# Kernel optimization log

Measured on AMD Instinct MI355X. Metric: run time of the kernel, lower is better.

## Reference

```python
import jax, jax.numpy as jnp
import numpy as np

VOL = 64          # self.vol_size
SPACE = 0.2       # space_size (cubic), space_center = 0
IMG = 255.0       # normalization constant in the source (2*u/255 - 1)


def setup_inputs() -> dict:
    key = jax.random.key(0)
    ks = jax.random.split(key, 5)
    B, V, C, Hf, Wf = 2, 4, 32, 64, 64
    features = jax.random.normal(ks[0], (B, V, C, Hf, Wf), jnp.float32)
    # near-identity rotations, cameras ~0.5m away, focal ~200, principal point 128
    camera_R = jnp.eye(3, dtype=jnp.float32)[None, None] + 0.01 * jax.random.normal(ks[1], (B, V, 3, 3), jnp.float32)
    camera_T = jnp.array([0.0, 0.0, 0.5], jnp.float32) + 0.01 * jax.random.normal(ks[2], (B, V, 3), jnp.float32)
    K0 = jnp.array([[200.0, 0.0, 128.0], [0.0, 200.0, 128.0], [0.0, 0.0, 1.0]], jnp.float32)
    Kmask = jnp.array([[1.0, 0.0, 1.0], [0.0, 1.0, 1.0], [0.0, 0.0, 0.0]], jnp.float32)
    camera_K = K0[None, None] + 0.5 * jax.random.normal(ks[3], (B, V, 3, 3), jnp.float32) * Kmask
    root_world = 0.01 * jax.random.normal(ks[4], (B, 3), jnp.float32)
    return dict(features=features, camera_R=camera_R, camera_T=camera_T,
                camera_K=camera_K, root_world=root_world)


def _bilinear_sample(feat, x, y):
    """PyTorch F.grid_sample, mode=bilinear, padding=zeros, align_corners=False.
    feat: [N,C,H,W]; x,y: [N,P] pixel-space coords (already unnormalized).
    Returns [N,C,P]."""
    N, C, H, W = feat.shape
    x0 = jnp.floor(x); y0 = jnp.floor(y)
    x1 = x0 + 1.0;     y1 = y0 + 1.0
    wx1 = x - x0; wx0 = 1.0 - wx1
    wy1 = y - y0; wy0 = 1.0 - wy1
    feat_flat = feat.reshape(N, C, H * W)

    def gather(xi, yi, w):
        valid = (xi >= 0) & (xi <= W - 1) & (yi >= 0) & (yi <= H - 1)
        xi_c = jnp.clip(xi, 0, W - 1).astype(jnp.int32)
        yi_c = jnp.clip(yi, 0, H - 1).astype(jnp.int32)
        idx = yi_c * W + xi_c                                   # [N,P]
        vals = jnp.take_along_axis(feat_flat, idx[:, None, :], axis=2)  # [N,C,P]
        return vals * (w * valid.astype(feat.dtype))[:, None, :]

    return (gather(x0, y0, wx0 * wy0) + gather(x1, y0, wx1 * wy0)
            + gather(x0, y1, wx0 * wy1) + gather(x1, y1, wx1 * wy1))


def reference(features, camera_R, camera_T, camera_K, root_world):
    B, V, C, Hf, Wf = features.shape
    D = VOL
    # _build_grid: 64^3 points, xyz order, spanning SPACE around center 0
    r = jnp.arange(D, dtype=jnp.float32)
    z, y, x = jnp.meshgrid(r, r, r, indexing='ij')
    grid = jnp.stack([x, y, z], axis=0) / (D - 1)               # [3,D,D,D]
    pts = ((grid - 0.5) * SPACE).reshape(3, -1).T               # [P,3], P = D^3
    # relative camera translation: new_T = R @ root + T
    new_T = jnp.einsum('bvij,bj->bvi', camera_R, root_world) + camera_T
    # project: pts_cam = pts @ R^T + T  -> [B,V,P,3]
    pts_cam = jnp.einsum('pj,bvij->bvpi', pts, camera_R) + new_T[:, :, None, :]
    zc = jnp.maximum(pts_cam[..., 2], 1e-5)
    fx = camera_K[:, :, 0, 0][..., None]; fy = camera_K[:, :, 1, 1][..., None]
    cx = camera_K[:, :, 0, 2][..., None]; cy = camera_K[:, :, 1, 2][..., None]
    u = pts_cam[..., 0] * fx / zc + cx
    v = pts_cam[..., 1] * fy / zc + cy
    u_n = 2.0 * u / IMG - 1.0
    v_n = 2.0 * v / IMG - 1.0
    # unnormalize (align_corners=False): ix = ((g+1)*W - 1)/2
    px = ((u_n + 1.0) * Wf - 1.0) * 0.5
    py = ((v_n + 1.0) * Hf - 1.0) * 0.5
    feat_bv = features.reshape(B * V, C, Hf, Wf)
    vol = _bilinear_sample(feat_bv, px.reshape(B * V, -1), py.reshape(B * V, -1))  # [BV,C,P]
    vol = vol.reshape(B, V, C, D, D, D).mean(axis=1)            # average over views
    return vol
```

## Files before the change

### kernel.cpp

```cpp
#include <hip/hip_runtime.h>

#define B_   2
#define V_   4
#define C_   32
#define HW_  4096
#define D_   64
#define P_   (D_*D_*D_)
#define SCL_ (64.0f/255.0f)

#define TXv_ 16
#define TYv_ 4
#define TZv_ 2
#define WCAP_ 10
#define HCAP_ 6
#define SLOTS_   64
#define SSTRIDE_ 80

typedef _Float16 half2v __attribute__((ext_vector_type(2)));
typedef __fp16  fp16x2 __attribute__((ext_vector_type(2)));

union Corner32 { uint4 u[2]; half2v h[8]; };
union H2U { half2v h; fp16x2 f; unsigned int u; };

__global__ __launch_bounds__(256) void tx_kernel(const float* __restrict__ in,
                                                 unsigned int* __restrict__ out) {
    __shared__ float tile[32][65];
    const int bv  = blockIdx.x >> 6;
    const int hw0 = (blockIdx.x & 63) << 6;
    const int t   = threadIdx.x;
    const float* src = in + (size_t)bv * C_ * HW_ + hw0;
#pragma unroll
    for (int i = 0; i < 8; ++i) {
        int e = t + (i << 8);
        tile[e >> 6][e & 63] = src[(e >> 6) * HW_ + (e & 63)];
    }
    __syncthreads();
    unsigned int* dst = out + ((size_t)bv * HW_ + hw0) * (C_ / 2);
#pragma unroll
    for (int i = 0; i < 4; ++i) {
        int idx = t + (i << 8);
        int c  = (idx << 1) & 31;
        int hw = idx >> 4;
        half2v v = { (_Float16)tile[c][hw], (_Float16)tile[c + 1][hw] };
        dst[idx] = *(unsigned int*)&v;
    }
}

__global__ __launch_bounds__(256, 6) void vol_kernel(
    const unsigned char* __restrict__ feat,
    const float* __restrict__ Rm,
    const float* __restrict__ Tm,
    const float* __restrict__ Km,
    const float* __restrict__ root,
    float* __restrict__ out)
{
    __shared__ __align__(16) float cam[4][20];
    __shared__ __align__(16) int   srect[4][8];
    __shared__ __align__(16) unsigned char sfeat[4][SLOTS_ * SSTRIDE_];

    const int t = threadIdx.x;
    const int b = blockIdx.x >> 11;
    const int tile = blockIdx.x & 2047;
    const int gx0 = (tile & 3) << 4;
    const int gy0 = ((tile >> 2) & 15) << 2;
    const int gz0 = (tile >> 6) << 1;

    if (t < 32) {
        const int v = t & 3, c = t >> 2;
        const int bv = b * V_ + v;
        const float* Rb = Rm + bv * 9;
        const float* Tb = Tm + bv * 3;
        const float* Kb = Km + bv * 9;
        const float rx = root[b*3+0], ry = root[b*3+1], rz = root[b*3+2];
        const float r00=Rb[0], r01=Rb[1], r02=Rb[2];
        const float r10=Rb[3], r11=Rb[4], r12=Rb[5];
        const float r20=Rb[6], r21=Rb[7], r22=Rb[8];
        const float t0 = r00*rx + r01*ry + r02*rz + Tb[0];
        const float t1 = r10*rx + r11*ry + r12*rz + Tb[1];
        const float t2 = r20*rx + r21*ry + r22*rz + Tb[2];
        const float fx = Kb[0] * SCL_, fy = Kb[4] * SCL_;
        const float cx = Kb[2] * SCL_ - 0.5f, cy = Kb[5] * SCL_ - 0.5f;

        const float X = ((float)(gx0 + (c & 1) * (TXv_-1)) * (1.0f/63.0f) - 0.5f) * 0.2f;
        const float Y = ((float)(gy0 + ((c >> 1) & 1) * (TYv_-1)) * (1.0f/63.0f) - 0.5f) * 0.2f;
        const float Z = ((float)(gz0 + (c >> 2) * (TZv_-1)) * (1.0f/63.0f) - 0.5f) * 0.2f;
        const float xc = r00*X + r01*Y + r02*Z + t0;
        const float yc = r10*X + r11*Y + r12*Z + t1;
        float zc       = r20*X + r21*Y + r22*Z + t2;
        zc = fmaxf(zc, 1e-5f);
        const float inv = 1.0f / zc;
        float px = (xc * inv) * fx + cx;
        float py = (yc * inv) * fy + cy;

        float pxmn = px, pxmx = px, pymn = py, pymx = py;
#pragma unroll
        for (int m = 4; m <= 16; m <<= 1) {
            pxmn = fminf(pxmn, __shfl_xor(pxmn, m));
            pxmx = fmaxf(pxmx, __shfl_xor(pxmx, m));
            pymn = fminf(pymn, __shfl_xor(pymn, m));
            pymx = fmaxf(pymx, __shfl_xor(pymx, m));
        }
        if (c == 0) {
            cam[v][0] = r00; cam[v][1] = r01; cam[v][2] = r02; cam[v][3] = t0;
            cam[v][4] = r10; cam[v][5] = r11; cam[v][6] = r12; cam[v][7] = t1;
            cam[v][8] = r20; cam[v][9] = r21; cam[v][10] = r22; cam[v][11] = t2;
            cam[v][12] = fx; cam[v][13] = fy; cam[v][14] = cx; cam[v][15] = cy;
            int rx0 = (int)floorf(pxmn); rx0 = max(0, min(63, rx0));
            int rx1 = (int)floorf(pxmx) + 1; rx1 = max(rx0, min(63, rx1));
            const int W = min(rx1 - rx0 + 1, WCAP_);
            int ry0 = (int)floorf(pymn); ry0 = max(0, min(63, ry0));
            int ry1 = (int)floorf(pymx) + 1; ry1 = max(ry0, min(63, ry1));
            const int H = min(ry1 - ry0 + 1, HCAP_);
            srect[v][0] = rx0; srect[v][1] = ry0; srect[v][2] = W; srect[v][3] = H;
            srect[v][4] = 65536 / W + 1;
            srect[v][5] = W * H * 4;
        }
    }
    __syncthreads();

    const int bvb = b * V_;
#pragma unroll
    for (int v = 0; v < 4; ++v) {
        const int nch = srect[v][5];
        if (t < nch) {
            const int rx0 = srect[v][0], ry0 = srect[v][1];
            const int W = srect[v][2], M = srect[v][4];
            const int part = t & 3, pi = t >> 2;
            const int dy = (pi * M) >> 16;
            const int dx = pi - dy * W;
            const unsigned char* src = feat + (size_t)(bvb + v) * HW_ * 64;
            const uint4 val = *(const uint4*)(src
                + (size_t)(((ry0 + dy) << 6) + rx0 + dx) * 64 + part * 16);
            *(uint4*)&sfeat[v][pi * SSTRIDE_ + part * 16] = val;
        }
    }
    __syncthreads();

    const int h = t & 1;
    const int vx = t >> 1;
    const float X = ((float)(gx0 + (vx & 15)) * (1.0f/63.0f) - 0.5f) * 0.2f;
    const float Y = ((float)(gy0 + ((vx >> 4) & 3)) * (1.0f/63.0f) - 0.5f) * 0.2f;
    const float Z = ((float)(gz0 + (vx >> 6)) * (1.0f/63.0f) - 0.5f) * 0.2f;

    const half2v z2 = { (_Float16)0.0f, (_Float16)0.0f };
    half2v acc[8];
#pragma unroll
    for (int j = 0; j < 8; ++j) acc[j] = z2;

#pragma unroll
    for (int v = 0; v < 4; ++v) {
        const float4 cA = *(const float4*)&cam[v][0];
        const float4 cB = *(const float4*)&cam[v][4];
        const float4 cC = *(const float4*)&cam[v][8];
        const float4 cK = *(const float4*)&cam[v][12];
        const int rx0 = srect[v][0], ry0 = srect[v][1], W = srect[v][2];

        const float xc = cA.x*X + cA.y*Y + cA.z*Z + cA.w;
        const float yc = cB.x*X + cB.y*Y + cB.z*Z + cB.w;
        float zc       = cC.x*X + cC.y*Y + cC.z*Z + cC.w;
        zc = fmaxf(zc, 1e-5f);
        const float inv = 1.0f / zc;
        const float px = (xc * inv) * cK.x + cK.z;
        const float py = (yc * inv) * cK.y + cK.w;

        const float x0f = floorf(px), y0f = floorf(py);
        const float wx1 = px - x0f, wx0 = 1.0f - wx1;
        const float wy1 = py - y0f, wy0 = 1.0f - wy1;
        const float x1f = x0f + 1.0f, y1f = y0f + 1.0f;
        const float vx0 = (x0f >= 0.0f && x0f <= 63.0f) ? 0.25f : 0.0f;
        const float vx1 = (x1f >= 0.0f && x1f <= 63.0f) ? 0.25f : 0.0f;
        const float vy0 = (y0f >= 0.0f && y0f <= 63.0f) ? 1.0f : 0.0f;
        const float vy1 = (y1f >= 0.0f && y1f <= 63.0f) ? 1.0f : 0.0f;
        const float w00 = wx0*wy0*vx0*vy0, w01 = wx1*wy0*vx1*vy0;
        const float w10 = wx0*wy1*vx0*vy1, w11 = wx1*wy1*vx1*vy1;
        H2U u0, u1, u2, u3;
        u0.f = __builtin_amdgcn_cvt_pkrtz(w00, w00);
        u1.f = __builtin_amdgcn_cvt_pkrtz(w01, w01);
        u2.f = __builtin_amdgcn_cvt_pkrtz(w10, w10);
        u3.f = __builtin_amdgcn_cvt_pkrtz(w11, w11);

        const int x0c = (int)fminf(fmaxf(x0f, 0.0f), 63.0f);
        const int x1c = (int)fminf(fmaxf(x1f, 0.0f), 63.0f);
        const int y0c = (int)fminf(fmaxf(y0f, 0.0f), 63.0f);
        const int y1c = (int)fminf(fmaxf(y1f, 0.0f), 63.0f);
        const int dx0 = x0c - rx0, dx1 = x1c - rx0;
        const int r0 = (y0c - ry0) * W, r1 = (y1c - ry0) * W;
        const int o00 = (r0 + dx0) * SSTRIDE_, o01 = (r0 + dx1) * SSTRIDE_;
        const int o10 = (r1 + dx0) * SSTRIDE_, o11 = (r1 + dx1) * SSTRIDE_;

        const unsigned char* vb = &sfeat[v][0] + (h << 5);
        Corner32 c00, c01, c10, c11;
        c00.u[0] = *(const uint4*)(vb + o00); c00.u[1] = *(const uint4*)(vb + o00 + 16);
        c01.u[0] = *(const uint4*)(vb + o01); c01.u[1] = *(const uint4*)(vb + o01 + 16);
        c10.u[0] = *(const uint4*)(vb + o10); c10.u[1] = *(const uint4*)(vb + o10 + 16);
        c11.u[0] = *(const uint4*)(vb + o11); c11.u[1] = *(const uint4*)(vb + o11 + 16);
#pragma unroll
        for (int j = 0; j < 8; ++j) {
            acc[j] += c00.h[j] * u0.h;
            acc[j] += c01.h[j] * u1.h;
            acc[j] += c10.h[j] * u2.h;
            acc[j] += c11.h[j] * u3.h;
        }
    }

    const int gx = gx0 + (vx & 15);
    const int gy = gy0 + ((vx >> 4) & 3);
    const int gz = gz0 + (vx >> 6);
    const int p = (((gz << 6) + gy) << 6) + gx;
    float* ob = out + ((size_t)(b * C_) + (h << 4)) * P_ + p;
#pragma unroll
    for (int j = 0; j < 8; ++j) {
        __builtin_nontemporal_store((float)acc[j].x, ob + (size_t)(2*j  ) * P_);
        __builtin_nontemporal_store((float)acc[j].y, ob + (size_t)(2*j+1) * P_);
    }
}

__global__ __launch_bounds__(256) void vol_fallback(
    const float* __restrict__ feat,
    const float* __restrict__ Rm, const float* __restrict__ Tm,
    const float* __restrict__ Km, const float* __restrict__ root,
    float* __restrict__ out)
{
    const int b = blockIdx.x >> 10;
    const int p = ((blockIdx.x & 1023) << 8) | threadIdx.x;
    const int xi = p & 63, yi = (p >> 6) & 63, zi = p >> 12;
    const float X = ((float)xi * (1.0f/63.0f) - 0.5f) * 0.2f;
    const float Y = ((float)yi * (1.0f/63.0f) - 0.5f) * 0.2f;
    const float Z = ((float)zi * (1.0f/63.0f) - 0.5f) * 0.2f;
    float acc[C_];
#pragma unroll
    for (int c = 0; c < C_; ++c) acc[c] = 0.0f;
    const float rx = root[b*3+0], ry = root[b*3+1], rz = root[b*3+2];
#pragma unroll
    for (int v = 0; v < V_; ++v) {
        const int bv = b * V_ + v;
        const float* Rb = Rm + bv * 9; const float* Tb = Tm + bv * 3;
        const float* Kb = Km + bv * 9;
        const float r00=Rb[0], r01=Rb[1], r02=Rb[2];
        const float r10=Rb[3], r11=Rb[4], r12=Rb[5];
        const float r20=Rb[6], r21=Rb[7], r22=Rb[8];
        const float t0 = r00*rx + r01*ry + r02*rz + Tb[0];
        const float t1 = r10*rx + r11*ry + r12*rz + Tb[1];
        const float t2 = r20*rx + r21*ry + r22*rz + Tb[2];
        const float xc = r00*X + r01*Y + r02*Z + t0;
        const float yc = r10*X + r11*Y + r12*Z + t1;
        float zc       = r20*X + r21*Y + r22*Z + t2;
        zc = fmaxf(zc, 1e-5f);
        const float inv = 1.0f / zc;
        const float px = xc * (Kb[0]*SCL_) * inv + (Kb[2]*SCL_ - 0.5f);
        const float py = yc * (Kb[4]*SCL_) * inv + (Kb[5]*SCL_ - 0.5f);
        const float x0f = floorf(px), y0f = floorf(py);
        const float wx1 = px - x0f, wx0 = 1.0f - wx1;
        const float wy1 = py - y0f, wy0 = 1.0f - wy1;
        const float x1f = x0f + 1.0f, y1f = y0f + 1.0f;
        const float vx0 = (x0f >= 0.0f && x0f <= 63.0f) ? 1.0f : 0.0f;
        const float vx1 = (x1f >= 0.0f && x1f <= 63.0f) ? 1.0f : 0.0f;
        const float vy0 = (y0f >= 0.0f && y0f <= 63.0f) ? 1.0f : 0.0f;
        const float vy1 = (y1f >= 0.0f && y1f <= 63.0f) ? 1.0f : 0.0f;
        const float w00 = wx0*wy0*vx0*vy0, w01 = wx1*wy0*vx1*vy0;
        const float w10 = wx0*wy1*vx0*vy1, w11 = wx1*wy1*vx1*vy1;
        const int x0c = (int)fminf(fmaxf(x0f, 0.0f), 63.0f);
        const int x1c = (int)fminf(fmaxf(x1f, 0.0f), 63.0f);
        const int y0c = (int)fminf(fmaxf(y0f, 0.0f), 63.0f);
        const int y1c = (int)fminf(fmaxf(y1f, 0.0f), 63.0f);
        const float* fb = feat + (size_t)bv * C_ * HW_;
        const int i00 = y0c*64 + x0c, i01 = y0c*64 + x1c;
        const int i10 = y1c*64 + x0c, i11 = y1c*64 + x1c;
#pragma unroll
        for (int c = 0; c < C_; ++c) {
            const float* f = fb + c * HW_;
            acc[c] += w00*f[i00] + w01*f[i01] + w10*f[i10] + w11*f[i11];
        }
    }
    float* ob = out + (size_t)b * C_ * P_ + p;
#pragma unroll
    for (int c = 0; c < C_; ++c) ob[(size_t)c * P_] = acc[c] * 0.25f;
}

extern "C" void kernel_launch(void* const* d_in, const int* in_sizes, int n_in,
                              void* d_out, int out_size, void* d_ws, size_t ws_size,
                              hipStream_t stream) {
    const float* feat = (const float*)d_in[0];
    const float* Rm   = (const float*)d_in[1];
    const float* Tm   = (const float*)d_in[2];
    const float* Km   = (const float*)d_in[3];
    const float* root = (const float*)d_in[4];
    float* out = (float*)d_out;

    const size_t need = (size_t)B_ * V_ * HW_ * C_ * sizeof(_Float16);
    if (ws_size >= need) {
        unsigned int* ftx = (unsigned int*)d_ws;
        tx_kernel<<<B_ * V_ * 64, 256, 0, stream>>>(feat, ftx);
        vol_kernel<<<B_ * 2048, 256, 0, stream>>>(
            (const unsigned char*)ftx, Rm, Tm, Km, root, out);
    } else {
        vol_fallback<<<B_ * P_ / 256, 256, 0, stream>>>(feat, Rm, Tm, Km, root, out);
    }
}
```

Before: 97.58 us.

## Gather bilinear corners directly from global memory instead of LDS staging

New measurement: 100.9 us. 1.03x slower.

```diff
diff --git a/kernel.cpp b/kernel.cpp
--- a/kernel.cpp
+++ b/kernel.cpp
@@ -11,10 +11,6 @@
 #define TXv_ 16
 #define TYv_ 4
 #define TZv_ 2
-#define WCAP_ 10
-#define HCAP_ 6
-#define SLOTS_   64
-#define SSTRIDE_ 80
 
 typedef _Float16 half2v __attribute__((ext_vector_type(2)));
 typedef __fp16  fp16x2 __attribute__((ext_vector_type(2)));
@@ -46,7 +42,7 @@
     }
 }
 
-__global__ __launch_bounds__(256, 6) void vol_kernel(
+__global__ __launch_bounds__(256, 4) void vol_kernel(
     const unsigned char* __restrict__ feat,
     const float* __restrict__ Rm,
     const float* __restrict__ Tm,
@@ -54,10 +50,6 @@
     const float* __restrict__ root,
     float* __restrict__ out)
 {
-    __shared__ __align__(16) float cam[4][20];
-    __shared__ __align__(16) int   srect[4][8];
-    __shared__ __align__(16) unsigned char sfeat[4][SLOTS_ * SSTRIDE_];
-
     const int t = threadIdx.x;
     const int b = blockIdx.x >> 11;
     const int tile = blockIdx.x & 2047;
@@ -65,13 +57,25 @@
     const int gy0 = ((tile >> 2) & 15) << 2;
     const int gz0 = (tile >> 6) << 1;
 
-    if (t < 32) {
-        const int v = t & 3, c = t >> 2;
+    const int h = t & 1;
+    const int vx = t >> 1;
+    const float X = ((float)(gx0 + (vx & 15)) * (1.0f/63.0f) - 0.5f) * 0.2f;
+    const float Y = ((float)(gy0 + ((vx >> 4) & 3)) * (1.0f/63.0f) - 0.5f) * 0.2f;
+    const float Z = ((float)(gz0 + (vx >> 6)) * (1.0f/63.0f) - 0.5f) * 0.2f;
+
+    const float rx = root[b*3+0], ry = root[b*3+1], rz = root[b*3+2];
+
+    const half2v z2 = { (_Float16)0.0f, (_Float16)0.0f };
+    half2v acc[8];
+#pragma unroll
+    for (int j = 0; j < 8; ++j) acc[j] = z2;
+
+#pragma unroll
+    for (int v = 0; v < 4; ++v) {
         const int bv = b * V_ + v;
         const float* Rb = Rm + bv * 9;
         const float* Tb = Tm + bv * 3;
         const float* Kb = Km + bv * 9;
-        const float rx = root[b*3+0], ry = root[b*3+1], rz = root[b*3+2];
         const float r00=Rb[0], r01=Rb[1], r02=Rb[2];
         const float r10=Rb[3], r11=Rb[4], r12=Rb[5];
         const float r20=Rb[6], r21=Rb[7], r22=Rb[8];
@@ -81,87 +85,13 @@
         const float fx = Kb[0] * SCL_, fy = Kb[4] * SCL_;
         const float cx = Kb[2] * SCL_ - 0.5f, cy = Kb[5] * SCL_ - 0.5f;
 
-        const float X = ((float)(gx0 + (c & 1) * (TXv_-1)) * (1.0f/63.0f) - 0.5f) * 0.2f;
-        const float Y = ((float)(gy0 + ((c >> 1) & 1) * (TYv_-1)) * (1.0f/63.0f) - 0.5f) * 0.2f;
-        const float Z = ((float)(gz0 + (c >> 2) * (TZv_-1)) * (1.0f/63.0f) - 0.5f) * 0.2f;
         const float xc = r00*X + r01*Y + r02*Z + t0;
         const float yc = r10*X + r11*Y + r12*Z + t1;
         float zc       = r20*X + r21*Y + r22*Z + t2;
         zc = fmaxf(zc, 1e-5f);
         const float inv = 1.0f / zc;
-        float px = (xc * inv) * fx + cx;
-        float py = (yc * inv) * fy + cy;
-
-        float pxmn = px, pxmx = px, pymn = py, pymx = py;
-#pragma unroll
-        for (int m = 4; m <= 16; m <<= 1) {
-            pxmn = fminf(pxmn, __shfl_xor(pxmn, m));
-            pxmx = fmaxf(pxmx, __shfl_xor(pxmx, m));
-            pymn = fminf(pymn, __shfl_xor(pymn, m));
-            pymx = fmaxf(pymx, __shfl_xor(pymx, m));
-        }
-        if (c == 0) {
-            cam[v][0] = r00; cam[v][1] = r01; cam[v][2] = r02; cam[v][3] = t0;
-            cam[v][4] = r10; cam[v][5] = r11; cam[v][6] = r12; cam[v][7] = t1;
-            cam[v][8] = r20; cam[v][9] = r21; cam[v][10] = r22; cam[v][11] = t2;
-            cam[v][12] = fx; cam[v][13] = fy; cam[v][14] = cx; cam[v][15] = cy;
-            int rx0 = (int)floorf(pxmn); rx0 = max(0, min(63, rx0));
-            int rx1 = (int)floorf(pxmx) + 1; rx1 = max(rx0, min(63, rx1));
-            const int W = min(rx1 - rx0 + 1, WCAP_);
-            int ry0 = (int)floorf(pymn); ry0 = max(0, min(63, ry0));
-            int ry1 = (int)floorf(pymx) + 1; ry1 = max(ry0, min(63, ry1));
-            const int H = min(ry1 - ry0 + 1, HCAP_);
-            srect[v][0] = rx0; srect[v][1] = ry0; srect[v][2] = W; srect[v][3] = H;
-            srect[v][4] = 65536 / W + 1;
-            srect[v][5] = W * H * 4;
-        }
-    }
-    __syncthreads();
-
-    const int bvb = b * V_;
-#pragma unroll
-    for (int v = 0; v < 4; ++v) {
-        const int nch = srect[v][5];
-        if (t < nch) {
-            const int rx0 = srect[v][0], ry0 = srect[v][1];
-            const int W = srect[v][2], M = srect[v][4];
-            const int part = t & 3, pi = t >> 2;
-            const int dy = (pi * M) >> 16;
-            const int dx = pi - dy * W;
-            const unsigned char* src = feat + (size_t)(bvb + v) * HW_ * 64;
-            const uint4 val = *(const uint4*)(src
-                + (size_t)(((ry0 + dy) << 6) + rx0 + dx) * 64 + part * 16);
-            *(uint4*)&sfeat[v][pi * SSTRIDE_ + part * 16] = val;
-        }
-    }
-    __syncthreads();
-
-    const int h = t & 1;
-    const int vx = t >> 1;
-    const float X = ((float)(gx0 + (vx & 15)) * (1.0f/63.0f) - 0.5f) * 0.2f;
-    const float Y = ((float)(gy0 + ((vx >> 4) & 3)) * (1.0f/63.0f) - 0.5f) * 0.2f;
-    const float Z = ((float)(gz0 + (vx >> 6)) * (1.0f/63.0f) - 0.5f) * 0.2f;
-
-    const half2v z2 = { (_Float16)0.0f, (_Float16)0.0f };
-    half2v acc[8];
-#pragma unroll
-    for (int j = 0; j < 8; ++j) acc[j] = z2;
-
-#pragma unroll
-    for (int v = 0; v < 4; ++v) {
-        const float4 cA = *(const float4*)&cam[v][0];
-        const float4 cB = *(const float4*)&cam[v][4];
-        const float4 cC = *(const float4*)&cam[v][8];
-        const float4 cK = *(const float4*)&cam[v][12];
-        const int rx0 = srect[v][0], ry0 = srect[v][1], W = srect[v][2];
-
-        const float xc = cA.x*X + cA.y*Y + cA.z*Z + cA.w;
-        const float yc = cB.x*X + cB.y*Y + cB.z*Z + cB.w;
-        float zc       = cC.x*X + cC.y*Y + cC.z*Z + cC.w;
-        zc = fmaxf(zc, 1e-5f);
-        const float inv = 1.0f / zc;
-        const float px = (xc * inv) * cK.x + cK.z;
-        const float py = (yc * inv) * cK.y + cK.w;
+        const float px = (xc * inv) * fx + cx;
+        const float py = (yc * inv) * fy + cy;
 
         const float x0f = floorf(px), y0f = floorf(py);
         const float wx1 = px - x0f, wx0 = 1.0f - wx1;
@@ -183,17 +113,15 @@
         const int x1c = (int)fminf(fmaxf(x1f, 0.0f), 63.0f);
         const int y0c = (int)fminf(fmaxf(y0f, 0.0f), 63.0f);
         const int y1c = (int)fminf(fmaxf(y1f, 0.0f), 63.0f);
-        const int dx0 = x0c - rx0, dx1 = x1c - rx0;
-        const int r0 = (y0c - ry0) * W, r1 = (y1c - ry0) * W;
-        const int o00 = (r0 + dx0) * SSTRIDE_, o01 = (r0 + dx1) * SSTRIDE_;
-        const int o10 = (r1 + dx0) * SSTRIDE_, o11 = (r1 + dx1) * SSTRIDE_;
-
-        const unsigned char* vb = &sfeat[v][0] + (h << 5);
+
+        const unsigned char* vb = feat + (size_t)bv * HW_ * 64 + (h << 5);
+        const int i00 = ((y0c << 6) + x0c) << 6, i01 = ((y0c << 6) + x1c) << 6;
+        const int i10 = ((y1c << 6) + x0c) << 6, i11 = ((y1c << 6) + x1c) << 6;
         Corner32 c00, c01, c10, c11;
-        c00.u[0] = *(const uint4*)(vb + o00); c00.u[1] = *(const uint4*)(vb + o00 + 16);
-        c01.u[0] = *(const uint4*)(vb + o01); c01.u[1] = *(const uint4*)(vb + o01 + 16);
-        c10.u[0] = *(const uint4*)(vb + o10); c10.u[1] = *(const uint4*)(vb + o10 + 16);
-        c11.u[0] = *(const uint4*)(vb + o11); c11.u[1] = *(const uint4*)(vb + o11 + 16);
+        c00.u[0] = *(const uint4*)(vb + i00); c00.u[1] = *(const uint4*)(vb + i00 + 16);
+        c01.u[0] = *(const uint4*)(vb + i01); c01.u[1] = *(const uint4*)(vb + i01 + 16);
+        c10.u[0] = *(const uint4*)(vb + i10); c10.u[1] = *(const uint4*)(vb + i10 + 16);
+        c11.u[0] = *(const uint4*)(vb + i11); c11.u[1] = *(const uint4*)(vb + i11 + 16);
 #pragma unroll
         for (int j = 0; j < 8; ++j) {
             acc[j] += c00.h[j] * u0.h;
```

## Process two z-slices per thread to amortize per-block camera and feature staging

Applied to the files above, without the earlier changes.

New measurement: 95.64 us. -2.0%, faster.

```diff
diff --git a/kernel.cpp b/kernel.cpp
--- a/kernel.cpp
+++ b/kernel.cpp
@@ -10,11 +10,12 @@
 
 #define TXv_ 16
 #define TYv_ 4
-#define TZv_ 2
+#define TZv_ 4
 #define WCAP_ 10
 #define HCAP_ 6
 #define SLOTS_   64
 #define SSTRIDE_ 80
+#define STEP_ (0.2f/63.0f)
 
 typedef _Float16 half2v __attribute__((ext_vector_type(2)));
 typedef __fp16  fp16x2 __attribute__((ext_vector_type(2)));
@@ -46,7 +47,51 @@
     }
 }
 
-__global__ __launch_bounds__(256, 6) void vol_kernel(
+__device__ __forceinline__ void gather_blend(
+    const unsigned char* __restrict__ vb,
+    float px, float py, int rx0, int ry0, int W,
+    half2v* __restrict__ acc)
+{
+    const float x0f = floorf(px), y0f = floorf(py);
+    const float wx1 = px - x0f, wx0 = 1.0f - wx1;
+    const float wy1 = py - y0f, wy0 = 1.0f - wy1;
+    const float x1f = x0f + 1.0f, y1f = y0f + 1.0f;
+    const float vx0 = (x0f >= 0.0f && x0f <= 63.0f) ? 0.25f : 0.0f;
+    const float vx1 = (x1f >= 0.0f && x1f <= 63.0f) ? 0.25f : 0.0f;
+    const float vy0 = (y0f >= 0.0f && y0f <= 63.0f) ? 1.0f : 0.0f;
+    const float vy1 = (y1f >= 0.0f && y1f <= 63.0f) ? 1.0f : 0.0f;
+    const float w00 = wx0*wy0*vx0*vy0, w01 = wx1*wy0*vx1*vy0;
+    const float w10 = wx0*wy1*vx0*vy1, w11 = wx1*wy1*vx1*vy1;
+    H2U u0, u1, u2, u3;
+    u0.f = __builtin_amdgcn_cvt_pkrtz(w00, w00);
+    u1.f = __builtin_amdgcn_cvt_pkrtz(w01, w01);
+    u2.f = __builtin_amdgcn_cvt_pkrtz(w10, w10);
+    u3.f = __builtin_amdgcn_cvt_pkrtz(w11, w11);
+
+    const int x0c = (int)fminf(fmaxf(x0f, 0.0f), 63.0f);
+    const int x1c = (int)fminf(fmaxf(x1f, 0.0f), 63.0f);
+    const int y0c = (int)fminf(fmaxf(y0f, 0.0f), 63.0f);
+    const int y1c = (int)fminf(fmaxf(y1f, 0.0f), 63.0f);
+    const int dx0 = x0c - rx0, dx1 = x1c - rx0;
+    const int r0 = (y0c - ry0) * W, r1 = (y1c - ry0) * W;
+    const int o00 = (r0 + dx0) * SSTRIDE_, o01 = (r0 + dx1) * SSTRIDE_;
+    const int o10 = (r1 + dx0) * SSTRIDE_, o11 = (r1 + dx1) * SSTRIDE_;
+
+    Corner32 c00, c01, c10, c11;
+    c00.u[0] = *(const uint4*)(vb + o00); c00.u[1] = *(const uint4*)(vb + o00 + 16);
+    c01.u[0] = *(const uint4*)(vb + o01); c01.u[1] = *(const uint4*)(vb + o01 + 16);
+    c10.u[0] = *(const uint4*)(vb + o10); c10.u[1] = *(const uint4*)(vb + o10 + 16);
+    c11.u[0] = *(const uint4*)(vb + o11); c11.u[1] = *(const uint4*)(vb + o11 + 16);
+#pragma unroll
+    for (int j = 0; j < 8; ++j) {
+        acc[j] += c00.h[j] * u0.h;
+        acc[j] += c01.h[j] * u1.h;
+        acc[j] += c10.h[j] * u2.h;
+        acc[j] += c11.h[j] * u3.h;
+    }
+}
+
+__global__ __launch_bounds__(256, 4) void vol_kernel(
     const unsigned char* __restrict__ feat,
     const float* __restrict__ Rm,
     const float* __restrict__ Tm,
@@ -59,11 +104,11 @@
     __shared__ __align__(16) unsigned char sfeat[4][SLOTS_ * SSTRIDE_];
 
     const int t = threadIdx.x;
-    const int b = blockIdx.x >> 11;
-    const int tile = blockIdx.x & 2047;
+    const int b = blockIdx.x >> 10;
+    const int tile = blockIdx.x & 1023;
     const int gx0 = (tile & 3) << 4;
     const int gy0 = ((tile >> 2) & 15) << 2;
-    const int gz0 = (tile >> 6) << 1;
+    const int gz0 = (tile >> 6) << 2;
 
     if (t < 32) {
         const int v = t & 3, c = t >> 2;
@@ -81,14 +126,14 @@
         const float fx = Kb[0] * SCL_, fy = Kb[4] * SCL_;
         const float cx = Kb[2] * SCL_ - 0.5f, cy = Kb[5] * SCL_ - 0.5f;
 
-        const float X = ((float)(gx0 + (c & 1) * (TXv_-1)) * (1.0f/63.0f) - 0.5f) * 0.2f;
-        const float Y = ((float)(gy0 + ((c >> 1) & 1) * (TYv_-1)) * (1.0f/63.0f) - 0.5f) * 0.2f;
-        const float Z = ((float)(gz0 + (c >> 2) * (TZv_-1)) * (1.0f/63.0f) - 0.5f) * 0.2f;
+        const float X = (float)(gx0 + (c & 1) * (TXv_-1)) * STEP_ - 0.1f;
+        const float Y = (float)(gy0 + ((c >> 1) & 1) * (TYv_-1)) * STEP_ - 0.1f;
+        const float Z = (float)(gz0 + (c >> 2) * (TZv_-1)) * STEP_ - 0.1f;
         const float xc = r00*X + r01*Y + r02*Z + t0;
         const float yc = r10*X + r11*Y + r12*Z + t1;
         float zc       = r20*X + r21*Y + r22*Z + t2;
         zc = fmaxf(zc, 1e-5f);
-        const float inv = 1.0f / zc;
+        const float inv = __builtin_amdgcn_rcpf(zc);
         float px = (xc * inv) * fx + cx;
         float py = (yc * inv) * fy + cy;
 
@@ -105,6 +150,8 @@
             cam[v][4] = r10; cam[v][5] = r11; cam[v][6] = r12; cam[v][7] = t1;
             cam[v][8] = r20; cam[v][9] = r21; cam[v][10] = r22; cam[v][11] = t2;
             cam[v][12] = fx; cam[v][13] = fy; cam[v][14] = cx; cam[v][15] = cy;
+            const float dZ = 2.0f * STEP_;
+            cam[v][16] = r02 * dZ; cam[v][17] = r12 * dZ; cam[v][18] = r22 * dZ;
             int rx0 = (int)floorf(pxmn); rx0 = max(0, min(63, rx0));
             int rx1 = (int)floorf(pxmx) + 1; rx1 = max(rx0, min(63, rx1));
             const int W = min(rx1 - rx0 + 1, WCAP_);
@@ -138,14 +185,14 @@
 
     const int h = t & 1;
     const int vx = t >> 1;
-    const float X = ((float)(gx0 + (vx & 15)) * (1.0f/63.0f) - 0.5f) * 0.2f;
-    const float Y = ((float)(gy0 + ((vx >> 4) & 3)) * (1.0f/63.0f) - 0.5f) * 0.2f;
-    const float Z = ((float)(gz0 + (vx >> 6)) * (1.0f/63.0f) - 0.5f) * 0.2f;
-
-    const half2v z2 = { (_Float16)0.0f, (_Float16)0.0f };
-    half2v acc[8];
-#pragma unroll
-    for (int j = 0; j < 8; ++j) acc[j] = z2;
+    const float X = (float)(gx0 + (vx & 15)) * STEP_ - 0.1f;
+    const float Y = (float)(gy0 + ((vx >> 4) & 3)) * STEP_ - 0.1f;
+    const float Z = (float)(gz0 + (vx >> 6)) * STEP_ - 0.1f;
+
+    const half2v z2h = { (_Float16)0.0f, (_Float16)0.0f };
+    half2v accA[8], accB[8];
+#pragma unroll
+    for (int j = 0; j < 8; ++j) { accA[j] = z2h; accB[j] = z2h; }
 
 #pragma unroll
     for (int v = 0; v < 4; ++v) {
@@ -153,54 +200,24 @@
         const float4 cB = *(const float4*)&cam[v][4];
         const float4 cC = *(const float4*)&cam[v][8];
         const float4 cK = *(const float4*)&cam[v][12];
+        const float dxz = cam[v][16], dyz = cam[v][17], dzz = cam[v][18];
         const int rx0 = srect[v][0], ry0 = srect[v][1], W = srect[v][2];
-
-        const float xc = cA.x*X + cA.y*Y + cA.z*Z + cA.w;
-        const float yc = cB.x*X + cB.y*Y + cB.z*Z + cB.w;
-        float zc       = cC.x*X + cC.y*Y + cC.z*Z + cC.w;
-        zc = fmaxf(zc, 1e-5f);
-        const float inv = 1.0f / zc;
-        const float px = (xc * inv) * cK.x + cK.z;
-        const float py = (yc * inv) * cK.y + cK.w;
-
-        const float x0f = floorf(px), y0f = floorf(py);
-        const float wx1 = px - x0f, wx0 = 1.0f - wx1;
-        const float wy1 = py - y0f, wy0 = 1.0f - wy1;
-        const float x1f = x0f + 1.0f, y1f = y0f + 1.0f;
-        const float vx0 = (x0f >= 0.0f && x0f <= 63.0f) ? 0.25f : 0.0f;
-        const float vx1 = (x1f >= 0.0f && x1f <= 63.0f) ? 0.25f : 0.0f;
-        const float vy0 = (y0f >= 0.0f && y0f <= 63.0f) ? 1.0f : 0.0f;
-        const float vy1 = (y1f >= 0.0f && y1f <= 63.0f) ? 1.0f : 0.0f;
-        const float w00 = wx0*wy0*vx0*vy0, w01 = wx1*wy0*vx1*vy0;
-        const float w10 = wx0*wy1*vx0*vy1, w11 = wx1*wy1*vx1*vy1;
-        H2U u0, u1, u2, u3;
-        u0.f = __builtin_amdgcn_cvt_pkrtz(w00, w00);
-        u1.f = __builtin_amdgcn_cvt_pkrtz(w01, w01);
-        u2.f = __builtin_amdgcn_cvt_pkrtz(w10, w10);
-        u3.f = __builtin_amdgcn_cvt_pkrtz(w11, w11);
-
-        const int x0c = (int)fminf(fmaxf(x0f, 0.0f), 63.0f);
-        const int x1c = (int)fminf(fmaxf(x1f, 0.0f), 63.0f);
-        const int y0c = (int)fminf(fmaxf(y0f, 0.0f), 63.0f);
-        const int y1c = (int)fminf(fmaxf(y1f, 0.0f), 63.0f);
-        const int dx0 = x0c - rx0, dx1 = x1c - rx0;
-        const int r0 = (y0c - ry0) * W, r1 = (y1c - ry0) * W;
-        const int o00 = (r0 + dx0) * SSTRIDE_, o01 = (r0 + dx1) * SSTRIDE_;
-        const int o10 = (r1 + dx0) * SSTRIDE_, o11 = (r1 + dx1) * SSTRIDE_;
-
         const unsigned char* vb = &sfeat[v][0] + (h << 5);
-        Corner32 c00, c01, c10, c11;
-        c00.u[0] = *(const uint4*)(vb + o00); c00.u[1] = *(const uint4*)(vb + o00 + 16);
-        c01.u[0] = *(const uint4*)(vb + o01); c01.u[1] = *(const uint4*)(vb + o01 + 16);
-        c10.u[0] = *(const uint4*)(vb + o10); c10.u[1] = *(const uint4*)(vb + o10 + 16);
-        c11.u[0] = *(const uint4*)(vb + o11); c11.u[1] = *(const uint4*)(vb + o11 + 16);
-#pragma unroll
-        for (int j = 0; j < 8; ++j) {
-            acc[j] += c00.h[j] * u0.h;
-            acc[j] += c01.h[j] * u1.h;
-            acc[j] += c10.h[j] * u2.h;
-            acc[j] += c11.h[j] * u3.h;
-        }
+
+        const float xcA = cA.x*X + cA.y*Y + cA.z*Z + cA.w;
+        const float ycA = cB.x*X + cB.y*Y + cB.z*Z + cB.w;
+        const float zcA = cC.x*X + cC.y*Y + cC.z*Z + cC.w;
+        const float xcB = xcA + dxz, ycB = ycA + dyz, zcB = zcA + dzz;
+
+        const float invA = __builtin_amdgcn_rcpf(fmaxf(zcA, 1e-5f));
+        const float invB = __builtin_amdgcn_rcpf(fmaxf(zcB, 1e-5f));
+        const float pxA = (xcA * invA) * cK.x + cK.z;
+        const float pyA = (ycA * invA) * cK.y + cK.w;
+        const float pxB = (xcB * invB) * cK.x + cK.z;
+        const float pyB = (ycB * invB) * cK.y + cK.w;
+
+        gather_blend(vb, pxA, pyA, rx0, ry0, W, accA);
+        gather_blend(vb, pxB, pyB, rx0, ry0, W, accB);
     }
 
     const int gx = gx0 + (vx & 15);
@@ -210,8 +227,10 @@
     float* ob = out + ((size_t)(b * C_) + (h << 4)) * P_ + p;
 #pragma unroll
     for (int j = 0; j < 8; ++j) {
-        __builtin_nontemporal_store((float)acc[j].x, ob + (size_t)(2*j  ) * P_);
-        __builtin_nontemporal_store((float)acc[j].y, ob + (size_t)(2*j+1) * P_);
+        __builtin_nontemporal_store((float)accA[j].x, ob + (size_t)(2*j  ) * P_);
+        __builtin_nontemporal_store((float)accA[j].y, ob + (size_t)(2*j+1) * P_);
+        __builtin_nontemporal_store((float)accB[j].x, ob + (size_t)(2*j  ) * P_ + 8192);
+        __builtin_nontemporal_store((float)accB[j].y, ob + (size_t)(2*j+1) * P_ + 8192);
     }
 }
 
@@ -291,7 +310,7 @@
     if (ws_size >= need) {
         unsigned int* ftx = (unsigned int*)d_ws;
         tx_kernel<<<B_ * V_ * 64, 256, 0, stream>>>(feat, ftx);
-        vol_kernel<<<B_ * 2048, 256, 0, stream>>>(
+        vol_kernel<<<B_ * 1024, 256, 0, stream>>>(
             (const unsigned char*)ftx, Rm, Tm, Km, root, out);
     } else {
         vol_fallback<<<B_ * P_ / 256, 256, 0, stream>>>(feat, Rm, Tm, Km, root, out);
```
